# Kernel optimization log

Hardware: AMD Instinct MI355X
Metric: run time of the kernel (lower is better)

The kernel has to match this reference:

```python
import jax, jax.numpy as jnp
import numpy as np

HID = 1024      # hidden_size (embedding dim, GRU input)
RNN = 1024      # rnn_hidden_size
VOCAB = 50000   # max_node
STEPS = 1024    # num_steps
SOS = 0


def setup_inputs() -> dict:
    key = jax.random.key(0)
    ks = jax.random.split(key, 8)
    s = 0.02
    return {
        "inputs": jax.random.randint(ks[0], (STEPS,), 0, VOCAB),
        "z": jax.random.normal(ks[1], (RNN,), jnp.float32),
        "emb_W": jax.random.uniform(ks[2], (VOCAB, HID), jnp.float32, -0.001, 0.001),
        "out_b": jnp.full((VOCAB,), 0.01, jnp.float32),
        "h2e_W": jax.random.normal(ks[3], (HID, RNN), jnp.float32) * s,
        "h2e_b": jnp.full((HID,), 0.01, jnp.float32),
        "W_ih": jax.random.normal(ks[4], (3 * RNN, HID), jnp.float32) * s,
        "W_hh": jax.random.normal(ks[5], (3 * RNN, RNN), jnp.float32) * s,
        "b_ih": jnp.zeros((3 * RNN,), jnp.float32),
        "b_hh": jnp.zeros((3 * RNN,), jnp.float32),
    }


def reference(inputs, z, emb_W, out_b, h2e_W, h2e_b, W_ih, W_hh, b_ih, b_hh):
    R = RNN

    def gru_cell(h, x):
        gi = W_ih @ x + b_ih          # (3R,)
        gh = W_hh @ h + b_hh          # (3R,)
        r = jax.nn.sigmoid(gi[:R] + gh[:R])
        zg = jax.nn.sigmoid(gi[R:2 * R] + gh[R:2 * R])
        n = jnp.tanh(gi[2 * R:] + r * gh[2 * R:])
        return (1.0 - zg) * n + zg * h

    # teacher forcing: step i consumes token_{i-1} (SOS for i=1), target is inputs[i]
    step_tokens = jnp.concatenate([jnp.array([SOS], dtype=inputs.dtype), inputs[1:-1]])
    targets = inputs[1:]

    def step(h, tok_tgt):
        tok, tgt = tok_tgt
        x = emb_W[tok]                              # embedding lookup (HID,)
        h_new = gru_cell(h, x)                      # (RNN,)
        e = h2e_W @ h_new + h2e_b                   # (HID,)
        logp = jax.nn.log_softmax(emb_W @ e + out_b)  # tied weights, (VOCAB,)
        return h_new, (-logp[tgt], jnp.argmax(logp))

    _, (losses, preds) = jax.lax.scan(step, z, (step_tokens, targets))
    loss = jnp.sum(losses)
    outputs = jnp.zeros((1, inputs.shape[0]), dtype=jnp.int32).at[0, 1:].set(preds.astype(jnp.int32))
    return loss, outputs
```

## Files before the change

### kernel.cpp

```cpp
#include <hip/hip_runtime.h>
#include <math.h>

#define NV      50000
#define T_STEPS 1023
#define KDIM    1024
#define NCH     391
#define TAU     4e-5f
#define NWL     320
typedef unsigned long long ull;


__global__ __launch_bounds__(256) void k_gemm_ffd(const int* __restrict__ inputs,
                                                  const float* __restrict__ emb,
                                                  const float* __restrict__ B,
                                                  const float* __restrict__ bias,
                                                  double* __restrict__ C,
                                                  int N, int K) {
  __shared__ float As[32][68];
  __shared__ float Bs[32][68];
  const int tid = threadIdx.x;
  const int bx = blockIdx.x, by = blockIdx.y;
  const int lr = tid >> 2;
  const int lk = (tid & 3) * 8;
  const int arow = by * 64 + lr;
  const int tok = (arow == 0) ? 0 : ((arow < T_STEPS) ? inputs[arow] : -1);
  const float* Ap = emb + (size_t)(tok < 0 ? 0 : tok) * K + lk;
  const float* Bp = B + (size_t)(bx * 64 + lr) * K + lk;
  const int r0 = (tid >> 4) * 4;
  const int c0 = (tid & 15) * 4;
  double acc[4][4] = {};
  for (int kc = 0; kc < K; kc += 32) {
    float4 a0 = make_float4(0.f, 0.f, 0.f, 0.f);
    float4 a1 = make_float4(0.f, 0.f, 0.f, 0.f);
    if (tok >= 0) { a0 = *(const float4*)(Ap + kc); a1 = *(const float4*)(Ap + kc + 4); }
    const float4 b0 = *(const float4*)(Bp + kc);
    const float4 b1 = *(const float4*)(Bp + kc + 4);
    __syncthreads();
    As[lk+0][lr]=a0.x; As[lk+1][lr]=a0.y; As[lk+2][lr]=a0.z; As[lk+3][lr]=a0.w;
    As[lk+4][lr]=a1.x; As[lk+5][lr]=a1.y; As[lk+6][lr]=a1.z; As[lk+7][lr]=a1.w;
    Bs[lk+0][lr]=b0.x; Bs[lk+1][lr]=b0.y; Bs[lk+2][lr]=b0.z; Bs[lk+3][lr]=b0.w;
    Bs[lk+4][lr]=b1.x; Bs[lk+5][lr]=b1.y; Bs[lk+6][lr]=b1.z; Bs[lk+7][lr]=b1.w;
    __syncthreads();
#pragma unroll
    for (int kk = 0; kk < 32; ++kk) {
      const float4 av = *(const float4*)&As[kk][r0];
      const float4 bv = *(const float4*)&Bs[kk][c0];
      const double aa[4] = {av.x, av.y, av.z, av.w};
      const double bb[4] = {bv.x, bv.y, bv.z, bv.w};
#pragma unroll
      for (int i = 0; i < 4; ++i)
#pragma unroll
        for (int j = 0; j < 4; ++j)
          acc[i][j] = fma(aa[i], bb[j], acc[i][j]);
    }
  }
  const int row = by * 64 + r0;
  const int col = bx * 64 + c0;
#pragma unroll
  for (int i = 0; i < 4; ++i)
#pragma unroll
    for (int j = 0; j < 4; ++j)
      C[(size_t)(row + i) * N + col + j] = acc[i][j] + (double)bias[col + j];
}

__global__ __launch_bounds__(256) void k_gemm_dfd(const double* __restrict__ A,
                                                  const float* __restrict__ B,
                                                  const float* __restrict__ bias,
                                                  double* __restrict__ C,
                                                  float* __restrict__ Cf,
                                                  int N, int K) {
  __shared__ double As[32][68];
  __shared__ float  Bs[32][68];
  const int tid = threadIdx.x;
  const int bx = blockIdx.x, by = blockIdx.y;
  const int lr = tid >> 2;
  const int lk = (tid & 3) * 8;
  const double* Ap = A + (size_t)(by * 64 + lr) * K + lk;
  const float*  Bp = B + (size_t)(bx * 64 + lr) * K + lk;
  const int r0 = (tid >> 4) * 4;
  const int c0 = (tid & 15) * 4;
  double acc[4][4] = {};
  for (int kc = 0; kc < K; kc += 32) {
    double ar[8];
#pragma unroll
    for (int q = 0; q < 8; ++q) ar[q] = Ap[kc + q];
    const float4 b0 = *(const float4*)(Bp + kc);
    const float4 b1 = *(const float4*)(Bp + kc + 4);
    __syncthreads();
#pragma unroll
    for (int q = 0; q < 8; ++q) As[lk + q][lr] = ar[q];
    Bs[lk+0][lr]=b0.x; Bs[lk+1][lr]=b0.y; Bs[lk+2][lr]=b0.z; Bs[lk+3][lr]=b0.w;
    Bs[lk+4][lr]=b1.x; Bs[lk+5][lr]=b1.y; Bs[lk+6][lr]=b1.z; Bs[lk+7][lr]=b1.w;
    __syncthreads();
#pragma unroll
    for (int kk = 0; kk < 32; ++kk) {
      const double aa[4] = {As[kk][r0+0], As[kk][r0+1], As[kk][r0+2], As[kk][r0+3]};
      const float4 bv = *(const float4*)&Bs[kk][c0];
      const double bb[4] = {bv.x, bv.y, bv.z, bv.w};
#pragma unroll
      for (int i = 0; i < 4; ++i)
#pragma unroll
        for (int j = 0; j < 4; ++j)
          acc[i][j] = fma(aa[i], bb[j], acc[i][j]);
    }
  }
  const int row = by * 64 + r0;
  const int col = bx * 64 + c0;
#pragma unroll
  for (int i = 0; i < 4; ++i)
#pragma unroll
    for (int j = 0; j < 4; ++j) {
      const double o = acc[i][j] + (double)bias[col + j];
      C [(size_t)(row + i) * N + col + j] = o;
      Cf[(size_t)(row + i) * N + col + j] = (float)o;
    }
}

__global__ __launch_bounds__(512, 2) void k_recur(const float* __restrict__ z,
                                                  const float* __restrict__ Whh,
                                                  const float* __restrict__ bhh,
                                                  const double* __restrict__ GI,
                                                  double* H, ull* ST) {
  __shared__ double hs[1024];
  const int tid = threadIdx.x;
  const int w = tid >> 6, l = tid & 63;
  const int ibase = blockIdx.x * 16 + w * 2;
  float wreg[6][16];
#pragma unroll
  for (int il = 0; il < 2; ++il)
#pragma unroll
    for (int g = 0; g < 3; ++g) {
      const float* wp = Whh + (size_t)(g * 1024 + ibase + il) * 1024 + l;
#pragma unroll
      for (int m = 0; m < 16; ++m) wreg[il * 3 + g][m] = wp[m * 64];
    }
  double bh[6];
#pragma unroll
  for (int il = 0; il < 2; ++il)
#pragma unroll
    for (int g = 0; g < 3; ++g) bh[il * 3 + g] = (double)bhh[g * 1024 + ibase + il];

  hs[tid]       = (double)z[tid];
  hs[tid + 512] = (double)z[tid + 512];
  double gi[6];
#pragma unroll
  for (int il = 0; il < 2; ++il)
#pragma unroll
    for (int g = 0; g < 3; ++g) gi[il * 3 + g] = GI[g * 1024 + ibase + il];
  __syncthreads();

  for (int t = 0; t < T_STEPS; ++t) {
    const bool more = (t + 1 < T_STEPS);
    double s[6] = {0.0, 0.0, 0.0, 0.0, 0.0, 0.0};
#pragma unroll
    for (int m = 0; m < 16; ++m) {
      const double hv = hs[l + 64 * m];
#pragma unroll
      for (int rr = 0; rr < 6; ++rr) s[rr] = fma((double)wreg[rr][m], hv, s[rr]);
    }
#pragma unroll
    for (int rr = 0; rr < 6; ++rr) {
      double v = s[rr];
#pragma unroll
      for (int mk = 32; mk >= 1; mk >>= 1) v += __shfl_xor(v, mk, 64);
      s[rr] = v;
    }
    double hn = 0.0;
    if (l < 2) {
      const int il = l;
      const double r  = 1.0 / (1.0 + exp(-(gi[il*3+0] + s[il*3+0] + bh[il*3+0])));
      const double zg = 1.0 / (1.0 + exp(-(gi[il*3+1] + s[il*3+1] + bh[il*3+1])));
      const double n  = tanh(gi[il*3+2] + r * (s[il*3+2] + bh[il*3+2]));
      hn = (1.0 - zg) * n + zg * hs[ibase + l];
    }
    double gin[6] = {0.0, 0.0, 0.0, 0.0, 0.0, 0.0};
    if (more) {
      const double* gp = GI + (size_t)(t + 1) * 3072;
#pragma unroll
      for (int il = 0; il < 2; ++il)
#pragma unroll
        for (int g = 0; g < 3; ++g) gin[il * 3 + g] = gp[g * 1024 + ibase + il];
    }
    __syncthreads();
    const ull tg = (ull)((t + 1) & 3);
    if (l < 2) {
      const int gidx = ibase + l;
      __hip_atomic_store(H + (size_t)t * 1024 + gidx, hn,
                         __ATOMIC_RELAXED, __HIP_MEMORY_SCOPE_AGENT);
      if (more) {
        const ull hb = (ull)__double_as_longlong(hn);
        __hip_atomic_store(ST + (size_t)((t + 1) & 1) * 1024 + gidx,
                           (hb & ~3ull) | tg,
                           __ATOMIC_RELAXED, __HIP_MEMORY_SCOPE_AGENT);
      }
    }
    if (more) {
      const ull* sp = ST + (size_t)((t + 1) & 1) * 1024 + 2 * tid;
      ull w0, w1;
      while (true) {
        w0 = __hip_atomic_load(sp,     __ATOMIC_RELAXED, __HIP_MEMORY_SCOPE_AGENT);
        w1 = __hip_atomic_load(sp + 1, __ATOMIC_RELAXED, __HIP_MEMORY_SCOPE_AGENT);
        if ((w0 & 3ull) == tg && (w1 & 3ull) == tg) break;
        __builtin_amdgcn_s_sleep(1);
      }
      hs[2 * tid]     = __longlong_as_double((long long)w0);
      hs[2 * tid + 1] = __longlong_as_double((long long)w1);
      __syncthreads();
#pragma unroll
      for (int q = 0; q < 6; ++q) gi[q] = gin[q];
    }
  }
}

__global__ __launch_bounds__(256) void k_logits_f32(
    const float* __restrict__ Ef, const double* __restrict__ E64,
    const float* __restrict__ emb, const float* __restrict__ out_b,
    const int* __restrict__ inputs,
    float* __restrict__ candL, int* __restrict__ candI,
    float* __restrict__ Psum, float* __restrict__ Ttgt) {
  __shared__ float As[128][33];
  __shared__ float Bs[32][132];
  __shared__ int   WLs[NWL];
  __shared__ int   WLv[NWL];
  __shared__ float Lr[NWL];
  __shared__ int   wcnt;
  const int tid = threadIdx.x;
  const int bx = blockIdx.x, by = blockIdx.y;
  const int wave = tid >> 6, lane = tid & 63;
  const int arow = tid >> 1, akk = (tid & 1) * 16;
  const float* Ap = Ef + (size_t)(by * 128 + arow) * KDIM + akk;
  const int bcol = tid >> 1, bk = (tid & 1) * 16;
  const int brow = bx * 128 + bcol;
  const float* Bp = emb + (size_t)brow * KDIM + bk;
  const bool bvalid = brow < NV;
  const int r0 = (tid >> 4) * 8;
  const int c0 = (tid & 15) * 8;
  float acc[8][8] = {};
  for (int kc = 0; kc < KDIM; kc += 32) {
    float4 ar[4], br[4];
#pragma unroll
    for (int q = 0; q < 4; ++q) {
      ar[q] = *(const float4*)(Ap + kc + q * 4);
      br[q] = bvalid ? *(const float4*)(Bp + kc + q * 4)
                     : make_float4(0.f, 0.f, 0.f, 0.f);
    }
    __syncthreads();
#pragma unroll
    for (int q = 0; q < 4; ++q) {
      As[arow][akk + q*4 + 0] = ar[q].x;
      As[arow][akk + q*4 + 1] = ar[q].y;
      As[arow][akk + q*4 + 2] = ar[q].z;
      As[arow][akk + q*4 + 3] = ar[q].w;
      Bs[bk + q*4 + 0][bcol] = br[q].x;
      Bs[bk + q*4 + 1][bcol] = br[q].y;
      Bs[bk + q*4 + 2][bcol] = br[q].z;
      Bs[bk + q*4 + 3][bcol] = br[q].w;
    }
    __syncthreads();
#pragma unroll 4
    for (int kk = 0; kk < 32; ++kk) {
      float aa[8];
#pragma unroll
      for (int i = 0; i < 8; ++i) aa[i] = As[r0 + i][kk];
      const float4 bv0 = *(const float4*)&Bs[kk][c0];
      const float4 bv1 = *(const float4*)&Bs[kk][c0 + 4];
      const float bb[8] = {bv0.x, bv0.y, bv0.z, bv0.w,
                           bv1.x, bv1.y, bv1.z, bv1.w};
#pragma unroll
      for (int i = 0; i < 8; ++i)
#pragma unroll
        for (int j = 0; j < 8; ++j)
          acc[i][j] = fmaf(aa[i], bb[j], acc[i][j]);
    }
  }
  const int colb = bx * 128 + c0;
  float ob[8];
#pragma unroll
  for (int j = 0; j < 8; ++j) {
    const int v = colb + j;
    ob[j] = (v < NV) ? out_b[v] : 0.f;
  }
#pragma unroll
  for (int i = 0; i < 8; ++i) {
    const int s = by * 128 + r0 + i;
    const bool valid = (s < T_STEPS);
    if (tid == 0) wcnt = 0;
    __syncthreads();
    float af[8];
    float M = -3e38f;
#pragma unroll
    for (int j = 0; j < 8; ++j) {
      const int v = colb + j;
      af[j] = (v < NV) ? acc[i][j] + ob[j] : -3e38f;
      M = fmaxf(M, af[j]);
    }
#pragma unroll
    for (int mk = 1; mk <= 8; mk <<= 1) M = fmaxf(M, __shfl_xor(M, mk, 64));
    int myidx[8];
#pragma unroll
    for (int j = 0; j < 8; ++j) {
      const int v = colb + j;
      myidx[j] = -1;
      if (valid && v < NV && af[j] >= M - TAU) {
        const int ix = atomicAdd(&wcnt, 1);
        if (ix < NWL) { myidx[j] = ix; WLs[ix] = s; WLv[ix] = v; }
        else myidx[j] = -2;
      }
    }
    __syncthreads();
    const int nw = min(wcnt, NWL);
    for (int wi = wave; wi < nw; wi += 4) {
      const int ss = WLs[wi], vv = WLv[wi];
      const double* Er = E64 + (size_t)ss * KDIM;
      const float*  br2 = emb + (size_t)vv * KDIM;
      double d = 0.0;
#pragma unroll
      for (int m = 0; m < 16; ++m)
        d = fma(Er[m * 64 + lane], (double)br2[m * 64 + lane], d);
#pragma unroll
      for (int mk = 32; mk >= 1; mk >>= 1) d += __shfl_xor(d, mk, 64);
      if (lane == 0) Lr[wi] = (float)(d + (double)out_b[vv]);
    }
    __syncthreads();
    float Lser[8];
#pragma unroll
    for (int j = 0; j < 8; ++j) {
      Lser[j] = -3e38f;
      if (myidx[j] == -2) {
        const double* Er = E64 + (size_t)s * KDIM;
        const float*  br2 = emb + (size_t)(colb + j) * KDIM;
        double d = 0.0;
        for (int k = 0; k < KDIM; ++k) d = fma(Er[k], (double)br2[k], d);
        Lser[j] = (float)(d + (double)out_b[colb + j]);
      }
    }
    const int tgt = valid ? inputs[s + 1] : -1;
    float L1 = -3e38f, L2 = -3e38f;
    int   i1 = 0x7FFFFFFF, i2 = 0x7FFFFFFF;
    float se = 0.f, tv = -INFINITY;
#pragma unroll
    for (int j = 0; j < 8; ++j) {
      const int v = colb + j;
      if (v < NV) {
        se += expf(af[j] - 0.01f);
        if (v == tgt) tv = af[j];
        const float L = (myidx[j] >= 0) ? Lr[myidx[j]]
                      : ((myidx[j] == -2) ? Lser[j] : -3e38f);
        if (L > L1 || (L == L1 && v < i1)) { L2 = L1; i2 = i1; L1 = L; i1 = v; }
        else if (L > L2 || (L == L2 && v < i2)) { L2 = L; i2 = v; }
      }
    }
#pragma unroll
    for (int mk = 1; mk <= 8; mk <<= 1) {
      const float oL1 = __shfl_xor(L1, mk, 64); const int oi1 = __shfl_xor(i1, mk, 64);
      const float oL2 = __shfl_xor(L2, mk, 64); const int oi2 = __shfl_xor(i2, mk, 64);
      if (oL1 > L1 || (oL1 == L1 && oi1 < i1)) { L2 = L1; i2 = i1; L1 = oL1; i1 = oi1; }
      else if (oL1 > L2 || (oL1 == L2 && oi1 < i2)) { L2 = oL1; i2 = oi1; }
      if (oL2 > L1 || (oL2 == L1 && oi2 < i1)) { L2 = L1; i2 = i1; L1 = oL2; i1 = oi2; }
      else if (oL2 > L2 || (oL2 == L2 && oi2 < i2)) { L2 = oL2; i2 = oi2; }
      se += __shfl_xor(se, mk, 64);
      tv = fmaxf(tv, __shfl_xor(tv, mk, 64));
    }
    if (((tid & 15) == 0) && valid) {
      const size_t p = (size_t)s * (2 * NCH) + 2 * bx;
      candL[p] = L1;     candI[p] = i1;
      candL[p + 1] = L2; candI[p + 1] = i2;
      atomicAdd(&Psum[s], se);
      if (tv > -1e30f) Ttgt[s] = tv;
    }
    __syncthreads();
  }
}

__global__ __launch_bounds__(256) void k_preds(const float* __restrict__ candL,
                                               const int* __restrict__ candI,
                                               float* __restrict__ out) {
  __shared__ float sL[256];
  __shared__ int   sI[256];
  const int s = blockIdx.x;
  const int tid = threadIdx.x;
  const int n = 2 * NCH;
  const size_t base = (size_t)s * n;
  float m = -3e38f;
  for (int c = tid; c < n; c += 256) m = fmaxf(m, candL[base + c]);
  sL[tid] = m; __syncthreads();
  for (int st = 128; st > 0; st >>= 1) {
    if (tid < st) sL[tid] = fmaxf(sL[tid], sL[tid + st]);
    __syncthreads();
  }
  const float Lmax = sL[0];
  __syncthreads();
  float bq = -3e38f; int bi = 0x7FFFFFFF;
  for (int c = tid; c < n; c += 256) {
    const float L = candL[base + c];
    const int   v = candI[base + c];
    const float d = L - Lmax;
    const float q = d - 10.8125f;
    if (q > bq || (q == bq && v < bi)) { bq = q; bi = v; }
  }
  sL[tid] = bq; sI[tid] = bi; __syncthreads();
  for (int st = 128; st > 0; st >>= 1) {
    if (tid < st) {
      if (sL[tid + st] > sL[tid] ||
          (sL[tid + st] == sL[tid] && sI[tid + st] < sI[tid])) {
        sL[tid] = sL[tid + st]; sI[tid] = sI[tid + st];
      }
    }
    __syncthreads();
  }
  if (tid == 0) out[2 + s] = (float)sI[0];
}

__global__ __launch_bounds__(1024) void k_finish(const float* __restrict__ Psum,
                                                 const float* __restrict__ Ttgt,
                                                 float* __restrict__ out) {
  __shared__ double red[1024];
  const int s = threadIdx.x;
  double ls = 0.0;
  if (s < T_STEPS) ls = 0.01 + log((double)Psum[s]) - (double)Ttgt[s];
  red[s] = ls;
  __syncthreads();
  for (int st = 512; st > 0; st >>= 1) {
    if (s < st) red[s] += red[s + st];
    __syncthreads();
  }
  if (s == 0) out[0] = (float)red[0];
  if (s == 1) out[1] = 0.f;
}

extern "C" void kernel_launch(void* const* d_in, const int* in_sizes, int n_in,
                              void* d_out, int out_size, void* d_ws, size_t ws_size,
                              hipStream_t stream) {
  const int*   inputs = (const int*)  d_in[0];
  const float* z      = (const float*)d_in[1];
  const float* emb    = (const float*)d_in[2];
  const float* out_b  = (const float*)d_in[3];
  const float* h2eW   = (const float*)d_in[4];
  const float* h2eb   = (const float*)d_in[5];
  const float* Wih    = (const float*)d_in[6];
  const float* Whh    = (const float*)d_in[7];
  const float* bih    = (const float*)d_in[8];
  const float* bhh    = (const float*)d_in[9];

  char* ws8 = (char*)d_ws;
  ull*    ST    = (ull*)ws8;
  float*  Psum  = (float*)(ws8 + 16384);
  float*  Ttgt  = (float*)(ws8 + 20480);
  char*   GIb   = ws8 + 49152;
  double* GI    = (double*)GIb;
  double* E     = GI;
  float*  candL = (float*)(GIb + (8u << 20));
  int*    candI = (int*)  (GIb + (8u << 20) + 3211264);
  float*  Ef    = (float*)(GIb + (8u << 20) + 6422528);
  double* H     = (double*)(GIb + (24u << 20));
  float*  out   = (float*)d_out;

  (void)hipMemsetAsync(ws8, 0, 24576, stream);

  k_gemm_ffd<<<dim3(48, 16), 256, 0, stream>>>(inputs, emb, Wih, bih, GI,
                                               3072, KDIM);
  k_recur<<<64, 512, 0, stream>>>(z, Whh, bhh, GI, H, ST);
  k_gemm_dfd<<<dim3(16, 16), 256, 0, stream>>>(H, h2eW, h2eb, E, Ef, KDIM, KDIM);
  k_logits_f32<<<dim3(NCH, 8), 256, 0, stream>>>(Ef, E, emb, out_b, inputs,
                                                 candL, candI, Psum, Ttgt);
  k_preds<<<T_STEPS, 256, 0, stream>>>(candL, candI, out);
  k_finish<<<1, 1024, 0, stream>>>(Psum, Ttgt, out);
}
```

Before: 9.643 ms.

## Carry full-precision hidden state in split tagged words with per-block done flags

```diff
diff --git a/kernel.cpp b/kernel.cpp
--- a/kernel.cpp
+++ b/kernel.cpp
@@ -120,7 +120,8 @@
                                                   const float* __restrict__ Whh,
                                                   const float* __restrict__ bhh,
                                                   const double* __restrict__ GI,
-                                                  double* H, ull* ST) {
+                                                  double* H, ull* SA, ull* SB,
+                                                  int* done) {
   __shared__ double hs[1024];
   const int tid = threadIdx.x;
   const int w = tid >> 6, l = tid & 63;
@@ -151,6 +152,12 @@
 
   for (int t = 0; t < T_STEPS; ++t) {
     const bool more = (t + 1 < T_STEPS);
+    const int p = t & 1;
+    const bool gate = more && (t >= 2);
+    int dv = 0x7FFFFFFF;
+    if (gate && tid < 64)
+      dv = __hip_atomic_load(done + p * 64 + tid,
+                             __ATOMIC_RELAXED, __HIP_MEMORY_SCOPE_AGENT);
     double s[6] = {0.0, 0.0, 0.0, 0.0, 0.0, 0.0};
 #pragma unroll
     for (int m = 0; m < 16; ++m) {
@@ -181,31 +188,54 @@
 #pragma unroll
         for (int g = 0; g < 3; ++g) gin[il * 3 + g] = gp[g * 1024 + ibase + il];
     }
-    __syncthreads();
-    const ull tg = (ull)((t + 1) & 3);
+    if (gate && tid < 64) {
+      while (!__all(dv >= t - 1)) {
+        __builtin_amdgcn_s_sleep(1);
+        dv = __hip_atomic_load(done + p * 64 + tid,
+                               __ATOMIC_RELAXED, __HIP_MEMORY_SCOPE_AGENT);
+      }
+    }
+    __syncthreads();
     if (l < 2) {
       const int gidx = ibase + l;
       __hip_atomic_store(H + (size_t)t * 1024 + gidx, hn,
                          __ATOMIC_RELAXED, __HIP_MEMORY_SCOPE_AGENT);
       if (more) {
-        const ull hb = (ull)__double_as_longlong(hn);
-        __hip_atomic_store(ST + (size_t)((t + 1) & 1) * 1024 + gidx,
-                           (hb & ~3ull) | tg,
+        const ull hb  = (ull)__double_as_longlong(hn);
+        const ull tag = ((ull)(t + 1)) << 32;
+        __hip_atomic_store(SA + p * 1024 + gidx, tag | (hb >> 32),
                            __ATOMIC_RELAXED, __HIP_MEMORY_SCOPE_AGENT);
+        __hip_atomic_store(SB + p * 1024 + gidx, tag | (hb & 0xFFFFFFFFull),
+                           __ATOMIC_RELAXED, __HIP_MEMORY_SCOPE_AGENT);
       }
     }
     if (more) {
-      const ull* sp = ST + (size_t)((t + 1) & 1) * 1024 + 2 * tid;
-      ull w0, w1;
+      const ull want = (ull)(t + 1);
+      ull a0, b0, a1, b1;
       while (true) {
-        w0 = __hip_atomic_load(sp,     __ATOMIC_RELAXED, __HIP_MEMORY_SCOPE_AGENT);
-        w1 = __hip_atomic_load(sp + 1, __ATOMIC_RELAXED, __HIP_MEMORY_SCOPE_AGENT);
-        if ((w0 & 3ull) == tg && (w1 & 3ull) == tg) break;
+        a0 = __hip_atomic_load(SA + p * 1024 + tid,
+                               __ATOMIC_RELAXED, __HIP_MEMORY_SCOPE_AGENT);
+        b0 = __hip_atomic_load(SB + p * 1024 + tid,
+                               __ATOMIC_RELAXED, __HIP_MEMORY_SCOPE_AGENT);
+        if ((a0 >> 32) >= want && (b0 >> 32) >= want) break;
         __builtin_amdgcn_s_sleep(1);
       }
-      hs[2 * tid]     = __longlong_as_double((long long)w0);
-      hs[2 * tid + 1] = __longlong_as_double((long long)w1);
+      while (true) {
+        a1 = __hip_atomic_load(SA + p * 1024 + tid + 512,
+                               __ATOMIC_RELAXED, __HIP_MEMORY_SCOPE_AGENT);
+        b1 = __hip_atomic_load(SB + p * 1024 + tid + 512,
+                               __ATOMIC_RELAXED, __HIP_MEMORY_SCOPE_AGENT);
+        if ((a1 >> 32) >= want && (b1 >> 32) >= want) break;
+        __builtin_amdgcn_s_sleep(1);
+      }
+      hs[tid]       = __longlong_as_double((long long)
+                        (((a0 & 0xFFFFFFFFull) << 32) | (b0 & 0xFFFFFFFFull)));
+      hs[tid + 512] = __longlong_as_double((long long)
+                        (((a1 & 0xFFFFFFFFull) << 32) | (b1 & 0xFFFFFFFFull)));
       __syncthreads();
+      if (tid == 0)
+        __hip_atomic_store(done + p * 64 + blockIdx.x, t + 1,
+                           __ATOMIC_RELAXED, __HIP_MEMORY_SCOPE_AGENT);
 #pragma unroll
       for (int q = 0; q < 6; ++q) gi[q] = gin[q];
     }
@@ -443,9 +473,11 @@
   const float* bhh    = (const float*)d_in[9];
 
   char* ws8 = (char*)d_ws;
-  ull*    ST    = (ull*)ws8;
-  float*  Psum  = (float*)(ws8 + 16384);
-  float*  Ttgt  = (float*)(ws8 + 20480);
+  ull*    SA    = (ull*)ws8;
+  ull*    SB    = (ull*)(ws8 + 16384);
+  int*    done  = (int*)(ws8 + 32768);
+  float*  Psum  = (float*)(ws8 + 33280);
+  float*  Ttgt  = (float*)(ws8 + 37376);
   char*   GIb   = ws8 + 49152;
   double* GI    = (double*)GIb;
   double* E     = GI;
@@ -455,11 +487,11 @@
   double* H     = (double*)(GIb + (24u << 20));
   float*  out   = (float*)d_out;
 
-  (void)hipMemsetAsync(ws8, 0, 24576, stream);
+  (void)hipMemsetAsync(ws8, 0, 49152, stream);
 
   k_gemm_ffd<<<dim3(48, 16), 256, 0, stream>>>(inputs, emb, Wih, bih, GI,
                                                3072, KDIM);
-  k_recur<<<64, 512, 0, stream>>>(z, Whh, bhh, GI, H, ST);
+  k_recur<<<64, 512, 0, stream>>>(z, Whh, bhh, GI, H, SA, SB, done);
   k_gemm_dfd<<<dim3(16, 16), 256, 0, stream>>>(H, h2eW, h2eb, E, Ef, KDIM, KDIM);
   k_logits_f32<<<dim3(NCH, 8), 256, 0, stream>>>(Ef, E, emb, out_b, inputs,
                                                  candL, candI, Psum, Ttgt);
```

Result: faster. 8.499 ms (-11.9%).
